# Kernel tuning notes

Measured on AMD Instinct MI355X. Metric: run time of the kernel, lower is better.

## Reference

```python
import jax, jax.numpy as jnp
import numpy as np

N = 50000      # nodes
E = 800000     # edges (avg degree 16)
F_IN = 64      # node_feature_dim
D = 128        # hidden_dim == output_dim
L = 3          # num_gnn_layers
B = 8          # number of graphs in the batch
GATE_H = 128   # GraphAttentionPool hidden_dim default


def _ln(x, g, b, eps=1e-5):
    m = x.mean(-1, keepdims=True)
    v = ((x - m) ** 2).mean(-1, keepdims=True)
    return (x - m) * jax.lax.rsqrt(v + eps) * g + b


def _gelu(x):
    return jax.nn.gelu(x, approximate=False)  # torch F.gelu default = exact erf


def setup_inputs() -> dict:
    key = jax.random.key(0)
    ks = jax.random.split(key, 12)
    p = lambda k, shape: (jax.random.normal(k, shape, jnp.float32) * 0.02)
    return {
        "x": jax.random.normal(ks[0], (N, F_IN), jnp.float32),
        "edge_index": jax.random.randint(ks[1], (2, E), 0, N, dtype=jnp.int32),
        "batch": jnp.sort(jax.random.randint(ks[2], (N,), 0, B, dtype=jnp.int32)),
        # input_proj: Linear + LayerNorm
        "w_in": p(ks[3], (F_IN, D)), "b_in": jnp.zeros((D,), jnp.float32),
        "ln_in_g": jnp.ones((D,), jnp.float32), "ln_in_b": jnp.zeros((D,), jnp.float32),
        # fallback GNN layers (stacked: all layers are 2D -> D)
        "gnn_w": p(ks[4], (L, 2 * D, D)), "gnn_b": jnp.zeros((L, D), jnp.float32),
        "gnn_ln_g": jnp.ones((L, D), jnp.float32), "gnn_ln_b": jnp.zeros((L, D), jnp.float32),
        # outer per-layer norms
        "norm_g": jnp.ones((L, D), jnp.float32), "norm_b": jnp.zeros((L, D), jnp.float32),
        # attention pool gate: Linear(D,128) -> tanh -> Linear(128,1)
        "gate_w1": p(ks[5], (D, GATE_H)), "gate_b1": jnp.zeros((GATE_H,), jnp.float32),
        "gate_w2": p(ks[6], (GATE_H,)), "gate_b2": jnp.zeros((), jnp.float32),
        # out_proj: Linear + LayerNorm + GELU
        "out_w": p(ks[7], (D, D)), "out_b": jnp.zeros((D,), jnp.float32),
        "out_ln_g": jnp.ones((D,), jnp.float32), "out_ln_b": jnp.zeros((D,), jnp.float32),
    }


def reference(x, edge_index, batch, w_in, b_in, ln_in_g, ln_in_b,
              gnn_w, gnn_b, gnn_ln_g, gnn_ln_b, norm_g, norm_b,
              gate_w1, gate_b1, gate_w2, gate_b2,
              out_w, out_b, out_ln_g, out_ln_b):
    src, dst = edge_index[0], edge_index[1]
    n = x.shape[0]

    # input_proj: Linear -> LayerNorm -> GELU
    h = _gelu(_ln(x @ w_in + b_in, ln_in_g, ln_in_b))

    # in-degree count (same every layer), clamped to >= 1
    deg = jax.ops.segment_sum(jnp.ones((src.shape[0],), h.dtype), dst, num_segments=n)
    deg = jnp.maximum(deg, 1.0)[:, None]  # (N, 1)

    for i in range(L):
        # mean-neighbor aggregation: gather x[src], scatter-add to dst
        agg = jax.ops.segment_sum(h[src], dst, num_segments=n) / deg  # (N, D)
        out = jnp.concatenate([h, agg], axis=-1) @ gnn_w[i] + gnn_b[i]
        h_new = _ln(_gelu(out), gnn_ln_g[i], gnn_ln_b[i])   # layer-internal norm
        h_new = _ln(h_new, norm_g[i], norm_b[i])             # outer norm
        if i < L - 1:
            h_new = _gelu(h_new) + h                         # residual (shapes match)
        h = h_new

    # attention pool (fallback path: global softmax over all nodes)
    gate_logits = jnp.tanh(h @ gate_w1 + gate_b1) @ gate_w2 + gate_b2  # (N,)
    gate = jax.nn.softmax(gate_logits, axis=0)
    pooled = jax.ops.segment_sum(h * gate[:, None], batch, num_segments=B)  # (B, D)

    spatial_embedding = _gelu(_ln(pooled @ out_w + out_b, out_ln_g, out_ln_b))
    return spatial_embedding, h, gate
```

## Files before the change

### kernel.cpp

```cpp
#include <hip/hip_runtime.h>
#include <math.h>

#define N_NODES 50000
#define N_EDGES 800000
#define F_IN 64
#define D 128
#define NLAYER 3
#define B_GRAPHS 8
#define GB 32
#define NPW 8
#define NBLK ((N_NODES + GB - 1) / GB)
#define SCAN_B 512
#define NPART ((N_NODES + SCAN_B - 1) / SCAN_B)
#define AGP 136

typedef float f32x4 __attribute__((ext_vector_type(4)));
typedef short bf16x8 __attribute__((ext_vector_type(8)));

__device__ __forceinline__ float gelu_exact(float x) {
    return 0.5f * x * (1.0f + erff(x * 0.7071067811865476f));
}

__device__ __forceinline__ unsigned short f2bf(float f) {
    unsigned int u = __float_as_uint(f);
    u = (u + 0x7fffu + ((u >> 16) & 1u)) >> 16;
    return (unsigned short)u;
}
__device__ __forceinline__ float bf2f(unsigned short u) {
    return __uint_as_float((unsigned int)u << 16);
}


__global__ void zero_int_kernel(int* __restrict__ p, int n) {
    int i = blockIdx.x * blockDim.x + threadIdx.x;
    int stride = gridDim.x * blockDim.x;
    for (; i < n; i += stride) p[i] = 0;
}

__global__ void degree_kernel(const int* __restrict__ dst, int* __restrict__ deg) {
    int e = blockIdx.x * blockDim.x + threadIdx.x;
    if (e < N_EDGES) atomicAdd(&deg[dst[e]], 1);
}

__global__ __launch_bounds__(SCAN_B) void scan_partials_kernel(const int* __restrict__ deg,
                                                               int* __restrict__ partials) {
    __shared__ int wsum[8];
    int tid = threadIdx.x;
    int lane = tid & 63, wave = tid >> 6;
    int i = blockIdx.x * SCAN_B + tid;
    int v = (i < N_NODES) ? deg[i] : 0;
    #pragma unroll
    for (int o = 32; o >= 1; o >>= 1) v += __shfl_xor(v, o);
    if (lane == 0) wsum[wave] = v;
    __syncthreads();
    if (tid == 0) {
        int t = 0;
        #pragma unroll
        for (int w = 0; w < 8; ++w) t += wsum[w];
        partials[blockIdx.x] = t;
    }
}

__global__ void scan_offsets_kernel(int* __restrict__ partials, int* __restrict__ row_ptr) {
    __shared__ int wtot[2];
    int tid = threadIdx.x;
    int lane = tid & 63, wave = tid >> 6;
    int v = (tid < NPART) ? partials[tid] : 0;
    int x = v;
    #pragma unroll
    for (int o = 1; o < 64; o <<= 1) { int nb = __shfl_up(x, o); if (lane >= o) x += nb; }
    if (lane == 63) wtot[wave] = x;
    __syncthreads();
    if (wave == 1) x += wtot[0];
    if (tid < NPART) partials[tid] = x - v;
    if (tid == 127) row_ptr[N_NODES] = x;
}

__global__ __launch_bounds__(SCAN_B) void scan_apply_kernel(const int* __restrict__ deg,
        const int* __restrict__ partials, int* __restrict__ row_ptr, int* __restrict__ cursor) {
    __shared__ int wsum[8];
    int tid = threadIdx.x;
    int lane = tid & 63, wave = tid >> 6;
    int i = blockIdx.x * SCAN_B + tid;
    int v = (i < N_NODES) ? deg[i] : 0;
    int x = v;
    #pragma unroll
    for (int o = 1; o < 64; o <<= 1) { int nb = __shfl_up(x, o); if (lane >= o) x += nb; }
    if (lane == 63) wsum[wave] = x;
    __syncthreads();
    int waveoff = 0;
    #pragma unroll
    for (int w = 0; w < 8; ++w) waveoff += (w < wave) ? wsum[w] : 0;
    int excl = partials[blockIdx.x] + waveoff + x - v;
    if (i < N_NODES) { row_ptr[i] = excl; cursor[i] = excl; }
}

__global__ void fill_kernel(const int* __restrict__ src, const int* __restrict__ dst,
                            int* __restrict__ cursor, int* __restrict__ csr) {
    int e = blockIdx.x * blockDim.x + threadIdx.x;
    if (e < N_EDGES) {
        int t = dst[e];
        int pos = atomicAdd(&cursor[t], 1);
        csr[pos] = src[e];
    }
}

#define WT_GNN (NLAYER * D * 2 * D)
#define WT_G1  (WT_GNN + D * D)
#define WT_ALL (WT_G1 + D * F_IN)
__global__ void wprep_kernel(const float* __restrict__ gnn_w, const float* __restrict__ gate_w1,
                             const float* __restrict__ w_in, unsigned short* __restrict__ wt,
                             float* __restrict__ pooled) {
    int idx = blockIdx.x * 256 + threadIdx.x;
    if (blockIdx.x == 0) {
        #pragma unroll
        for (int i = 0; i < 4; ++i) pooled[threadIdx.x + i * 256] = 0.f;
    }
    if (idx >= WT_ALL) return;
    if (idx < WT_GNN) {
        int l = idx / (D * 2 * D);
        int rem = idx - l * (D * 2 * D);
        int n = rem / (2 * D);
        int k = rem - n * (2 * D);
        wt[idx] = f2bf(gnn_w[(size_t)l * 2 * D * D + (size_t)k * D + n]);
    } else if (idx < WT_G1) {
        int rem = idx - WT_GNN;
        int n = rem / D;
        int k = rem - n * D;
        wt[idx] = f2bf(gate_w1[(size_t)k * D + n]);
    } else {
        int rem = idx - WT_G1;
        int n = rem / F_IN;
        int k = rem - n * F_IN;
        wt[idx] = f2bf(w_in[(size_t)k * D + n]);
    }
}


__global__ __launch_bounds__(256) void input_proj_v5(
        const float* __restrict__ x, const unsigned short* __restrict__ wti,
        const float* __restrict__ b, const float* __restrict__ gam,
        const float* __restrict__ bet, unsigned short* __restrict__ h16) {
    __shared__ float2 red[2][GB];
    int tid = threadIdx.x;
    int wave = tid >> 6, lane = tid & 63;
    int nblk0 = blockIdx.x * GB;
    int q = lane >> 4, c = lane & 15;
    int m0 = (wave >> 1) * 16;
    int n0 = (wave & 1) * 64;
    int mrow = nblk0 + m0 + c;
    int mclamp = (mrow < N_NODES) ? mrow : (N_NODES - 1);
    const float* xr = x + (size_t)mclamp * F_IN;

    f32x4 acc[4];
    #pragma unroll
    for (int t = 0; t < 4; ++t) {
        float bn = b[n0 + t * 16 + c];
        acc[t] = (f32x4){bn, bn, bn, bn};
    }
    #pragma unroll
    for (int kk = 0; kk < 2; ++kk) {
        float4 a0 = *(const float4*)&xr[kk * 32 + q * 8];
        float4 a1 = *(const float4*)&xr[kk * 32 + q * 8 + 4];
        bf16x8 av;
        av[0] = (short)f2bf(a0.x); av[1] = (short)f2bf(a0.y);
        av[2] = (short)f2bf(a0.z); av[3] = (short)f2bf(a0.w);
        av[4] = (short)f2bf(a1.x); av[5] = (short)f2bf(a1.y);
        av[6] = (short)f2bf(a1.z); av[7] = (short)f2bf(a1.w);
        #pragma unroll
        for (int t = 0; t < 4; ++t) {
            bf16x8 bv = *(const bf16x8*)&wti[(size_t)(n0 + t * 16 + c) * F_IN + kk * 32 + q * 8];
            acc[t] = __builtin_amdgcn_mfma_f32_16x16x32_bf16(av, bv, acc[t], 0, 0, 0);
        }
    }
    float s[4], sq[4];
    #pragma unroll
    for (int r = 0; r < 4; ++r) {
        s[r] = acc[0][r] + acc[1][r] + acc[2][r] + acc[3][r];
        sq[r] = acc[0][r] * acc[0][r] + acc[1][r] * acc[1][r]
              + acc[2][r] * acc[2][r] + acc[3][r] * acc[3][r];
    }
    #pragma unroll
    for (int o = 1; o <= 8; o <<= 1)
        #pragma unroll
        for (int r = 0; r < 4; ++r) { s[r] += __shfl_xor(s[r], o); sq[r] += __shfl_xor(sq[r], o); }
    if (c == 0) {
        #pragma unroll
        for (int r = 0; r < 4; ++r) red[wave & 1][m0 + q * 4 + r] = make_float2(s[r], sq[r]);
    }
    __syncthreads();
    float gv[4], bv2[4];
    #pragma unroll
    for (int t = 0; t < 4; ++t) {
        int nn = n0 + t * 16 + c;
        gv[t] = gam[nn]; bv2[t] = bet[nn];
    }
    #pragma unroll
    for (int r = 0; r < 4; ++r) {
        int m = m0 + q * 4 + r;
        int n = nblk0 + m;
        float2 p0 = red[0][m], p1 = red[1][m];
        float mean = (p0.x + p1.x) * (1.0f / D);
        float msq  = (p0.y + p1.y) * (1.0f / D);
        float istd = rsqrtf(msq - mean * mean + 1e-5f);
        if (n < N_NODES) {
            #pragma unroll
            for (int t = 0; t < 4; ++t) {
                int nn = n0 + t * 16 + c;
                float y = (acc[t][r] - mean) * istd * gv[t] + bv2[t];
                h16[(size_t)n * D + nn] = f2bf(gelu_exact(y));
            }
        }
    }
}


__device__ __forceinline__ void acc_row(float acc[8], bf16x8 v) {
    #pragma unroll
    for (int i = 0; i < 8; ++i)
        acc[i] += __uint_as_float(((unsigned int)(unsigned short)v[i]) << 16);
}

template<int DO_GATE>
__global__ __launch_bounds__(256) void gnn_layer_v7(
        const unsigned short* __restrict__ h16_in, unsigned short* __restrict__ h16_out,
        float* __restrict__ hf_out,
        const int* __restrict__ csr, const int* __restrict__ rp,
        const unsigned short* __restrict__ wt,
        const float* __restrict__ bias,
        const float* __restrict__ ln1g, const float* __restrict__ ln1b,
        const float* __restrict__ ln2g, const float* __restrict__ ln2b,
        int residual, int write_f32,
        const unsigned short* __restrict__ wtg,
        const float* __restrict__ gb1, const float* __restrict__ gw2,
        const float* __restrict__ gb2,
        float* __restrict__ logits, float2* __restrict__ gpart) {
    __shared__ int rps[GB + 1];
    __shared__ int eidx[GB][32];
    __shared__ unsigned short aggb[GB][AGP];
    __shared__ float2 red1[2][GB];
    __shared__ float2 red2[2][GB];
    __shared__ float redg[2][GB];
    __shared__ float lg[GB];

    int tid = threadIdx.x;
    int wave = tid >> 6, lane = tid & 63;
    int nblk0 = blockIdx.x * GB;
    int gbase = wave * NPW;

    if (tid < GB + 1) {
        int n = nblk0 + tid;
        if (n > N_NODES) n = N_NODES;
        rps[tid] = rp[n];
    }
    __syncthreads();
    #pragma unroll
    for (int k2 = 0; k2 < 4; ++k2) {
        int f = tid + k2 * 256;
        int g = f >> 5, sl = f & 31;
        int beg = rps[g], end = rps[g + 1];
        int ee = beg + sl;
        int ci = (ee < end) ? ee : ((end > beg) ? (end - 1) : 0);
        eidx[g][sl] = csr[ci];
    }
    __syncthreads();

    {
        int er = lane >> 4, dg = lane & 15;
        #pragma unroll
        for (int j = 0; j < NPW; ++j) {
            int g = gbase + j;
            int beg = rps[g], end = rps[g + 1];
            int deg = end - beg;
            int id8[8];
            #pragma unroll
            for (int t = 0; t < 8; ++t) id8[t] = eidx[g][er + 4 * t];
            bf16x8 v[8];
            #pragma unroll
            for (int t = 0; t < 8; ++t)
                v[t] = *(const bf16x8*)&h16_in[(size_t)id8[t] * D + dg * 8];
            float acc[8];
            #pragma unroll
            for (int i = 0; i < 8; ++i) acc[i] = 0.f;
            #pragma unroll
            for (int t = 0; t < 8; ++t)
                if (beg + er + 4 * t < end) acc_row(acc, v[t]);
            if (deg > 32) {
                for (int ee = beg + er + 32; ee < end; ee += 4) {
                    bf16x8 vv = *(const bf16x8*)&h16_in[(size_t)csr[ee] * D + dg * 8];
                    acc_row(acc, vv);
                }
            }
            #pragma unroll
            for (int i = 0; i < 8; ++i) {
                acc[i] += __shfl_xor(acc[i], 16);
                acc[i] += __shfl_xor(acc[i], 32);
            }
            float inv = 1.0f / fmaxf((float)deg, 1.0f);
            if (er == 0) {
                bf16x8 o;
                #pragma unroll
                for (int i = 0; i < 8; ++i) o[i] = (short)f2bf(acc[i] * inv);
                *(bf16x8*)&aggb[g][dg * 8] = o;
            }
        }
    }
    __syncthreads();

    int q = lane >> 4, c = lane & 15;
    int m0 = (wave >> 1) * 16;
    int n0 = (wave & 1) * 64;
    int mrow = nblk0 + m0 + c;
    int mclamp = (mrow < N_NODES) ? mrow : (N_NODES - 1);
    const unsigned short* arow = h16_in + (size_t)mclamp * D;

    f32x4 acc[4];
    #pragma unroll
    for (int t = 0; t < 4; ++t) {
        float bn = bias[n0 + t * 16 + c];
        acc[t] = (f32x4){bn, bn, bn, bn};
    }
    #pragma unroll
    for (int kk = 0; kk < 4; ++kk) {
        bf16x8 av = *(const bf16x8*)&arow[kk * 32 + q * 8];
        #pragma unroll
        for (int t = 0; t < 4; ++t) {
            bf16x8 bv = *(const bf16x8*)&wt[(size_t)(n0 + t * 16 + c) * 256 + kk * 32 + q * 8];
            acc[t] = __builtin_amdgcn_mfma_f32_16x16x32_bf16(av, bv, acc[t], 0, 0, 0);
        }
    }
    #pragma unroll
    for (int kk = 0; kk < 4; ++kk) {
        bf16x8 av = *(const bf16x8*)&aggb[m0 + c][kk * 32 + q * 8];
        #pragma unroll
        for (int t = 0; t < 4; ++t) {
            bf16x8 bv = *(const bf16x8*)&wt[(size_t)(n0 + t * 16 + c) * 256 + 128 + kk * 32 + q * 8];
            acc[t] = __builtin_amdgcn_mfma_f32_16x16x32_bf16(av, bv, acc[t], 0, 0, 0);
        }
    }

    float xv[4][4];
    #pragma unroll
    for (int t = 0; t < 4; ++t)
        #pragma unroll
        for (int r = 0; r < 4; ++r) xv[t][r] = gelu_exact(acc[t][r]);

    float s[4], sq[4];
    #pragma unroll
    for (int r = 0; r < 4; ++r) {
        s[r] = xv[0][r] + xv[1][r] + xv[2][r] + xv[3][r];
        sq[r] = xv[0][r] * xv[0][r] + xv[1][r] * xv[1][r] + xv[2][r] * xv[2][r] + xv[3][r] * xv[3][r];
    }
    #pragma unroll
    for (int o = 1; o <= 8; o <<= 1)
        #pragma unroll
        for (int r = 0; r < 4; ++r) { s[r] += __shfl_xor(s[r], o); sq[r] += __shfl_xor(sq[r], o); }
    int nh = wave & 1;
    if (c == 0) {
        #pragma unroll
        for (int r = 0; r < 4; ++r) red1[nh][m0 + q * 4 + r] = make_float2(s[r], sq[r]);
    }
    __syncthreads();

    float g1v[4], b1v[4], g2v[4], b2v[4];
    #pragma unroll
    for (int t = 0; t < 4; ++t) {
        int nn = n0 + t * 16 + c;
        g1v[t] = ln1g[nn]; b1v[t] = ln1b[nn];
        g2v[t] = ln2g[nn]; b2v[t] = ln2b[nn];
    }

    float y1[4][4];
    #pragma unroll
    for (int r = 0; r < 4; ++r) {
        int m = m0 + q * 4 + r;
        float2 p0 = red1[0][m], p1 = red1[1][m];
        float mean = (p0.x + p1.x) * (1.0f / D);
        float msq  = (p0.y + p1.y) * (1.0f / D);
        float istd = rsqrtf(msq - mean * mean + 1e-5f);
        #pragma unroll
        for (int t = 0; t < 4; ++t)
            y1[t][r] = (xv[t][r] - mean) * istd * g1v[t] + b1v[t];
    }

    #pragma unroll
    for (int r = 0; r < 4; ++r) {
        s[r] = y1[0][r] + y1[1][r] + y1[2][r] + y1[3][r];
        sq[r] = y1[0][r] * y1[0][r] + y1[1][r] * y1[1][r] + y1[2][r] * y1[2][r] + y1[3][r] * y1[3][r];
    }
    #pragma unroll
    for (int o = 1; o <= 8; o <<= 1)
        #pragma unroll
        for (int r = 0; r < 4; ++r) { s[r] += __shfl_xor(s[r], o); sq[r] += __shfl_xor(sq[r], o); }
    if (c == 0) {
        #pragma unroll
        for (int r = 0; r < 4; ++r) red2[nh][m0 + q * 4 + r] = make_float2(s[r], sq[r]);
    }
    __syncthreads();

    #pragma unroll
    for (int r = 0; r < 4; ++r) {
        int m = m0 + q * 4 + r;
        int n = nblk0 + m;
        float2 p0 = red2[0][m], p1 = red2[1][m];
        float mean = (p0.x + p1.x) * (1.0f / D);
        float msq  = (p0.y + p1.y) * (1.0f / D);
        float istd = rsqrtf(msq - mean * mean + 1e-5f);
        #pragma unroll
        for (int t = 0; t < 4; ++t) {
            int nn = n0 + t * 16 + c;
            float y2 = (y1[t][r] - mean) * istd * g2v[t] + b2v[t];
            float o = residual ? (gelu_exact(y2) + bf2f(h16_in[(size_t)n * D + nn])) : y2;
            if (n < N_NODES) {
                h16_out[(size_t)n * D + nn] = f2bf(o);
                if (write_f32) hf_out[(size_t)n * D + nn] = o;
            }
            if (DO_GATE) aggb[m][nn] = f2bf(o);
        }
    }

    if (DO_GATE) {
        __syncthreads();
        f32x4 gacc[4];
        #pragma unroll
        for (int t = 0; t < 4; ++t) {
            float bn = gb1[n0 + t * 16 + c];
            gacc[t] = (f32x4){bn, bn, bn, bn};
        }
        #pragma unroll
        for (int kk = 0; kk < 4; ++kk) {
            bf16x8 av = *(const bf16x8*)&aggb[m0 + c][kk * 32 + q * 8];
            #pragma unroll
            for (int t = 0; t < 4; ++t) {
                bf16x8 bv = *(const bf16x8*)&wtg[(size_t)(n0 + t * 16 + c) * 128 + kk * 32 + q * 8];
                gacc[t] = __builtin_amdgcn_mfma_f32_16x16x32_bf16(av, bv, gacc[t], 0, 0, 0);
            }
        }
        float w2v[4];
        #pragma unroll
        for (int t = 0; t < 4; ++t) w2v[t] = gw2[n0 + t * 16 + c];
        float gs[4];
        #pragma unroll
        for (int r = 0; r < 4; ++r) {
            gs[r] = tanhf(gacc[0][r]) * w2v[0] + tanhf(gacc[1][r]) * w2v[1]
                  + tanhf(gacc[2][r]) * w2v[2] + tanhf(gacc[3][r]) * w2v[3];
        }
        #pragma unroll
        for (int o = 1; o <= 8; o <<= 1)
            #pragma unroll
            for (int r = 0; r < 4; ++r) gs[r] += __shfl_xor(gs[r], o);
        if (c == 0) {
            #pragma unroll
            for (int r = 0; r < 4; ++r) redg[nh][m0 + q * 4 + r] = gs[r];
        }
        __syncthreads();
        if ((wave & 1) == 0 && c == 0) {
            float bb2 = gb2[0];
            #pragma unroll
            for (int r = 0; r < 4; ++r) {
                int m = m0 + q * 4 + r;
                int n = nblk0 + m;
                float L = redg[0][m] + redg[1][m] + bb2;
                if (n < N_NODES) { logits[n] = L; lg[m] = L; }
                else lg[m] = -INFINITY;
            }
        }
        __syncthreads();
        if (wave == 0) {
            float l = (lane < GB) ? lg[lane] : -INFINITY;
            float mx = l;
            #pragma unroll
            for (int o = 32; o >= 1; o >>= 1) mx = fmaxf(mx, __shfl_xor(mx, o));
            float ex = (lane < GB && l > -INFINITY) ? expf(l - mx) : 0.f;
            #pragma unroll
            for (int o = 32; o >= 1; o >>= 1) ex += __shfl_xor(ex, o);
            if (lane == 0) gpart[blockIdx.x] = make_float2(mx, ex);
        }
    }
}


#define POOL_CHUNK 128
__global__ __launch_bounds__(POOL_CHUNK) void gate_pool_v2(
        const unsigned short* __restrict__ h16, const float* __restrict__ logits,
        const float2* __restrict__ gpart, const int* __restrict__ batch,
        float* __restrict__ gate_out, float* __restrict__ pooled) {
    __shared__ float sb[4];
    __shared__ float gs[POOL_CHUNK];
    __shared__ int bs[POOL_CHUNK];
    int d = threadIdx.x;
    int lane = d & 63, wv = d >> 6;
    float mx = -INFINITY;
    for (int i = d; i < NBLK; i += POOL_CHUNK) mx = fmaxf(mx, gpart[i].x);
    #pragma unroll
    for (int o = 32; o >= 1; o >>= 1) mx = fmaxf(mx, __shfl_xor(mx, o));
    if (lane == 0) sb[wv] = mx;
    __syncthreads();
    mx = fmaxf(sb[0], sb[1]);
    float ssum = 0.f;
    for (int i = d; i < NBLK; i += POOL_CHUNK) {
        float2 p = gpart[i];
        ssum += p.y * expf(p.x - mx);
    }
    #pragma unroll
    for (int o = 32; o >= 1; o >>= 1) ssum += __shfl_xor(ssum, o);
    if (lane == 0) sb[2 + wv] = ssum;
    __syncthreads();
    float inv = 1.0f / (sb[2] + sb[3]);

    int n0 = blockIdx.x * POOL_CHUNK;
    int nj = n0 + d;
    if (nj < N_NODES) {
        float gv = expf(logits[nj] - mx) * inv;
        gs[d] = gv;
        bs[d] = batch[nj];
        gate_out[nj] = gv;
    }
    __syncthreads();
    int count = min(POOL_CHUNK, N_NODES - n0);
    float acc = 0.f;
    int cur = bs[0];
    int t = 0;
    for (; t + 3 < count; t += 4) {
        float h0 = bf2f(h16[(size_t)(n0 + t + 0) * D + d]);
        float h1 = bf2f(h16[(size_t)(n0 + t + 1) * D + d]);
        float h2 = bf2f(h16[(size_t)(n0 + t + 2) * D + d]);
        float h3 = bf2f(h16[(size_t)(n0 + t + 3) * D + d]);
        int b0 = bs[t], b1 = bs[t + 1], b2 = bs[t + 2], b3 = bs[t + 3];
        if (b0 != cur) { atomicAdd(&pooled[cur * D + d], acc); acc = 0.f; cur = b0; }
        acc = fmaf(h0, gs[t], acc);
        if (b1 != cur) { atomicAdd(&pooled[cur * D + d], acc); acc = 0.f; cur = b1; }
        acc = fmaf(h1, gs[t + 1], acc);
        if (b2 != cur) { atomicAdd(&pooled[cur * D + d], acc); acc = 0.f; cur = b2; }
        acc = fmaf(h2, gs[t + 2], acc);
        if (b3 != cur) { atomicAdd(&pooled[cur * D + d], acc); acc = 0.f; cur = b3; }
        acc = fmaf(h3, gs[t + 3], acc);
    }
    for (; t < count; ++t) {
        int bn = bs[t];
        if (bn != cur) { atomicAdd(&pooled[cur * D + d], acc); acc = 0.f; cur = bn; }
        acc = fmaf(bf2f(h16[(size_t)(n0 + t) * D + d]), gs[t], acc);
    }
    atomicAdd(&pooled[cur * D + d], acc);
}

__global__ void out_proj_kernel(const float* __restrict__ pooled, const float* __restrict__ w,
                                const float* __restrict__ b, const float* __restrict__ g,
                                const float* __restrict__ beta, float* __restrict__ emb) {
    __shared__ float ps[D];
    __shared__ float sbuf[2];
    int bg = blockIdx.x, d = threadIdx.x;
    ps[d] = pooled[bg * D + d];
    __syncthreads();
    float acc = b[d];
    #pragma unroll 8
    for (int k = 0; k < D; ++k) acc += ps[k] * w[k * D + d];
    float s = acc, q = acc * acc;
    #pragma unroll
    for (int o = 32; o >= 1; o >>= 1) { s += __shfl_down(s, o); q += __shfl_down(q, o); }
    if ((d & 63) == 0) { sbuf[d >> 6] = s; }
    __syncthreads();
    float fullsum = sbuf[0] + sbuf[1];
    __syncthreads();
    if ((d & 63) == 0) { sbuf[d >> 6] = q; }
    __syncthreads();
    float fullsq = sbuf[0] + sbuf[1];
    float m = fullsum * (1.0f / D);
    float var = fullsq * (1.0f / D) - m * m;
    float y = (acc - m) * rsqrtf(var + 1e-5f) * g[d] + beta[d];
    emb[bg * D + d] = gelu_exact(y);
}

extern "C" void kernel_launch(void* const* d_in, const int* in_sizes, int n_in,
                              void* d_out, int out_size, void* d_ws, size_t ws_size,
                              hipStream_t stream) {
    const float* x        = (const float*)d_in[0];
    const int*   edge     = (const int*)d_in[1];
    const int*   batch    = (const int*)d_in[2];
    const float* w_in     = (const float*)d_in[3];
    const float* b_in     = (const float*)d_in[4];
    const float* ln_in_g  = (const float*)d_in[5];
    const float* ln_in_b  = (const float*)d_in[6];
    const float* gnn_w    = (const float*)d_in[7];
    const float* gnn_b    = (const float*)d_in[8];
    const float* gnn_ln_g = (const float*)d_in[9];
    const float* gnn_ln_b = (const float*)d_in[10];
    const float* norm_g   = (const float*)d_in[11];
    const float* norm_b   = (const float*)d_in[12];
    const float* gate_w1  = (const float*)d_in[13];
    const float* gate_b1  = (const float*)d_in[14];
    const float* gate_w2  = (const float*)d_in[15];
    const float* gate_b2  = (const float*)d_in[16];
    const float* out_w    = (const float*)d_in[17];
    const float* out_b    = (const float*)d_in[18];
    const float* out_ln_g = (const float*)d_in[19];
    const float* out_ln_b = (const float*)d_in[20];

    const int* src = edge;
    const int* dst = edge + N_EDGES;

    float* out      = (float*)d_out;
    float* emb      = out;
    float* hA       = out + B_GRAPHS * D;
    float* gate_out = hA + (size_t)N_NODES * D;

    unsigned short* h16A = (unsigned short*)d_ws;
    unsigned short* h16B = h16A + (size_t)N_NODES * D;
    int*   deg_i    = (int*)d_ws;
    int*   cursor   = (int*)d_ws + N_NODES;
    int*   row_ptr  = (int*)(h16B + (size_t)N_NODES * D);
    int*   csr      = row_ptr + N_NODES + 1;
    float* logits   = (float*)(csr + N_EDGES);
    float* pooled   = logits + N_NODES;
    int*   partials = (int*)(pooled + B_GRAPHS * D);
    float2* gpart   = (float2*)(((uintptr_t)(partials + NPART) + 15) & ~(uintptr_t)15);
    unsigned short* wt  = (unsigned short*)(gpart + NBLK);
    unsigned short* wtg = wt + WT_GNN;
    unsigned short* wti = wt + WT_G1;

    zero_int_kernel<<<128, 256, 0, stream>>>(deg_i, N_NODES);
    degree_kernel<<<(N_EDGES + 255) / 256, 256, 0, stream>>>(dst, deg_i);
    scan_partials_kernel<<<NPART, SCAN_B, 0, stream>>>(deg_i, partials);
    scan_offsets_kernel<<<1, 128, 0, stream>>>(partials, row_ptr);
    scan_apply_kernel<<<NPART, SCAN_B, 0, stream>>>(deg_i, partials, row_ptr, cursor);
    fill_kernel<<<(N_EDGES + 255) / 256, 256, 0, stream>>>(src, dst, cursor, csr);
    wprep_kernel<<<(WT_ALL + 255) / 256, 256, 0, stream>>>(gnn_w, gate_w1, w_in, wt, pooled);

    input_proj_v5<<<NBLK, 256, 0, stream>>>(x, wti, b_in, ln_in_g, ln_in_b, h16B);

    gnn_layer_v7<0><<<NBLK, 256, 0, stream>>>(
        h16B, h16A, hA, csr, row_ptr, wt, gnn_b,
        gnn_ln_g, gnn_ln_b, norm_g, norm_b, 1, 0,
        nullptr, nullptr, nullptr, nullptr, nullptr, nullptr);
    gnn_layer_v7<0><<<NBLK, 256, 0, stream>>>(
        h16A, h16B, hA, csr, row_ptr, wt + (size_t)1 * D * 2 * D, gnn_b + D,
        gnn_ln_g + D, gnn_ln_b + D, norm_g + D, norm_b + D, 1, 0,
        nullptr, nullptr, nullptr, nullptr, nullptr, nullptr);
    gnn_layer_v7<1><<<NBLK, 256, 0, stream>>>(
        h16B, h16A, hA, csr, row_ptr, wt + (size_t)2 * D * 2 * D, gnn_b + 2 * D,
        gnn_ln_g + 2 * D, gnn_ln_b + 2 * D, norm_g + 2 * D, norm_b + 2 * D, 0, 1,
        wtg, gate_b1, gate_w2, gate_b2, logits, gpart);

    gate_pool_v2<<<(N_NODES + POOL_CHUNK - 1) / POOL_CHUNK, POOL_CHUNK, 0, stream>>>(
        h16A, logits, gpart, batch, gate_out, pooled);
    out_proj_kernel<<<B_GRAPHS, D, 0, stream>>>(pooled, out_w, out_b, out_ln_g, out_ln_b, emb);
}
```

Before: 455.6 us.

## Interleave two-node gathers, fuse scan offsets, memset degrees, halve pool chunk

The neighbor aggregation now processes two nodes per iteration, issuing both nodes' sixteen gathered row loads before accumulating, so more memory requests are in flight. The scan-offsets kernel is removed: each apply block sums the preceding partials itself, and block 0 writes the total. The zeroing kernel becomes a hipMemsetAsync. The gate-pool kernel uses 64-node chunks per block to double the block count. The price is more registers in the gather loop, which may lower occupancy, plus redundant partial sums in the scan.

New measurement: 458.8 us. Within noise of the previous version (+0.7%).

```diff
diff --git a/kernel.cpp b/kernel.cpp
--- a/kernel.cpp
+++ b/kernel.cpp
@@ -31,12 +31,6 @@
 }
 
 
-__global__ void zero_int_kernel(int* __restrict__ p, int n) {
-    int i = blockIdx.x * blockDim.x + threadIdx.x;
-    int stride = gridDim.x * blockDim.x;
-    for (; i < n; i += stride) p[i] = 0;
-}
-
 __global__ void degree_kernel(const int* __restrict__ dst, int* __restrict__ deg) {
     int e = blockIdx.x * blockDim.x + threadIdx.x;
     if (e < N_EDGES) atomicAdd(&deg[dst[e]], 1);
@@ -61,26 +55,45 @@
     }
 }
 
-__global__ void scan_offsets_kernel(int* __restrict__ partials, int* __restrict__ row_ptr) {
-    __shared__ int wtot[2];
+__global__ __launch_bounds__(SCAN_B) void scan_apply_v2(const int* __restrict__ deg,
+        const int* __restrict__ partials, int* __restrict__ row_ptr, int* __restrict__ cursor) {
+    __shared__ int wsum[8];
+    __shared__ int base_s;
     int tid = threadIdx.x;
     int lane = tid & 63, wave = tid >> 6;
-    int v = (tid < NPART) ? partials[tid] : 0;
-    int x = v;
-    #pragma unroll
-    for (int o = 1; o < 64; o <<= 1) { int nb = __shfl_up(x, o); if (lane >= o) x += nb; }
-    if (lane == 63) wtot[wave] = x;
-    __syncthreads();
-    if (wave == 1) x += wtot[0];
-    if (tid < NPART) partials[tid] = x - v;
-    if (tid == 127) row_ptr[N_NODES] = x;
-}
-
-__global__ __launch_bounds__(SCAN_B) void scan_apply_kernel(const int* __restrict__ deg,
-        const int* __restrict__ partials, int* __restrict__ row_ptr, int* __restrict__ cursor) {
-    __shared__ int wsum[8];
-    int tid = threadIdx.x;
-    int lane = tid & 63, wave = tid >> 6;
+
+    int b = 0;
+    for (int i = tid; i < (int)blockIdx.x; i += SCAN_B) b += partials[i];
+    #pragma unroll
+    for (int o = 32; o >= 1; o >>= 1) b += __shfl_xor(b, o);
+    if (lane == 0) wsum[wave] = b;
+    __syncthreads();
+    if (tid == 0) {
+        int t = 0;
+        #pragma unroll
+        for (int w = 0; w < 8; ++w) t += wsum[w];
+        base_s = t;
+    }
+    __syncthreads();
+    int base = base_s;
+    __syncthreads();
+
+    if (blockIdx.x == 0) {
+        int t = 0;
+        for (int i = tid; i < NPART; i += SCAN_B) t += partials[i];
+        #pragma unroll
+        for (int o = 32; o >= 1; o >>= 1) t += __shfl_xor(t, o);
+        if (lane == 0) wsum[wave] = t;
+        __syncthreads();
+        if (tid == 0) {
+            int tt = 0;
+            #pragma unroll
+            for (int w = 0; w < 8; ++w) tt += wsum[w];
+            row_ptr[N_NODES] = tt;
+        }
+        __syncthreads();
+    }
+
     int i = blockIdx.x * SCAN_B + tid;
     int v = (i < N_NODES) ? deg[i] : 0;
     int x = v;
@@ -91,7 +104,7 @@
     int waveoff = 0;
     #pragma unroll
     for (int w = 0; w < 8; ++w) waveoff += (w < wave) ? wsum[w] : 0;
-    int excl = partials[blockIdx.x] + waveoff + x - v;
+    int excl = base + waveoff + x - v;
     if (i < N_NODES) { row_ptr[i] = excl; cursor[i] = excl; }
 }
 
@@ -222,7 +235,7 @@
 }
 
 template<int DO_GATE>
-__global__ __launch_bounds__(256) void gnn_layer_v7(
+__global__ __launch_bounds__(256) void gnn_layer_v8(
         const unsigned short* __restrict__ h16_in, unsigned short* __restrict__ h16_out,
         float* __restrict__ hf_out,
         const int* __restrict__ csr, const int* __restrict__ rp,
@@ -268,40 +281,61 @@
     {
         int er = lane >> 4, dg = lane & 15;
         #pragma unroll
-        for (int j = 0; j < NPW; ++j) {
-            int g = gbase + j;
-            int beg = rps[g], end = rps[g + 1];
-            int deg = end - beg;
-            int id8[8];
-            #pragma unroll
-            for (int t = 0; t < 8; ++t) id8[t] = eidx[g][er + 4 * t];
-            bf16x8 v[8];
+        for (int jj = 0; jj < NPW; jj += 2) {
+            int gA = gbase + jj, gB2 = gbase + jj + 1;
+            int begA = rps[gA], endA = rps[gA + 1];
+            int begB = rps[gB2], endB = rps[gB2 + 1];
+            int degA = endA - begA, degB = endB - begB;
+            int idA[8], idB[8];
+            #pragma unroll
+            for (int t = 0; t < 8; ++t) { idA[t] = eidx[gA][er + 4 * t]; idB[t] = eidx[gB2][er + 4 * t]; }
+            bf16x8 vA[8], vB[8];
             #pragma unroll
             for (int t = 0; t < 8; ++t)
-                v[t] = *(const bf16x8*)&h16_in[(size_t)id8[t] * D + dg * 8];
-            float acc[8];
-            #pragma unroll
-            for (int i = 0; i < 8; ++i) acc[i] = 0.f;
+                vA[t] = *(const bf16x8*)&h16_in[(size_t)idA[t] * D + dg * 8];
             #pragma unroll
             for (int t = 0; t < 8; ++t)
-                if (beg + er + 4 * t < end) acc_row(acc, v[t]);
-            if (deg > 32) {
-                for (int ee = beg + er + 32; ee < end; ee += 4) {
+                vB[t] = *(const bf16x8*)&h16_in[(size_t)idB[t] * D + dg * 8];
+
+            float accA[8], accB[8];
+            #pragma unroll
+            for (int i = 0; i < 8; ++i) { accA[i] = 0.f; accB[i] = 0.f; }
+            #pragma unroll
+            for (int t = 0; t < 8; ++t)
+                if (begA + er + 4 * t < endA) acc_row(accA, vA[t]);
+            #pragma unroll
+            for (int t = 0; t < 8; ++t)
+                if (begB + er + 4 * t < endB) acc_row(accB, vB[t]);
+            if (degA > 32) {
+                for (int ee = begA + er + 32; ee < endA; ee += 4) {
                     bf16x8 vv = *(const bf16x8*)&h16_in[(size_t)csr[ee] * D + dg * 8];
-                    acc_row(acc, vv);
+                    acc_row(accA, vv);
                 }
             }
+            if (degB > 32) {
+                for (int ee = begB + er + 32; ee < endB; ee += 4) {
+                    bf16x8 vv = *(const bf16x8*)&h16_in[(size_t)csr[ee] * D + dg * 8];
+                    acc_row(accB, vv);
+                }
+            }
             #pragma unroll
             for (int i = 0; i < 8; ++i) {
-                acc[i] += __shfl_xor(acc[i], 16);
-                acc[i] += __shfl_xor(acc[i], 32);
-            }
-            float inv = 1.0f / fmaxf((float)deg, 1.0f);
+                accA[i] += __shfl_xor(accA[i], 16);
+                accA[i] += __shfl_xor(accA[i], 32);
+                accB[i] += __shfl_xor(accB[i], 16);
+                accB[i] += __shfl_xor(accB[i], 32);
+            }
+            float invA = 1.0f / fmaxf((float)degA, 1.0f);
+            float invB = 1.0f / fmaxf((float)degB, 1.0f);
             if (er == 0) {
-                bf16x8 o;
+                bf16x8 oA, oB;
                 #pragma unroll
-                for (int i = 0; i < 8; ++i) o[i] = (short)f2bf(acc[i] * inv);
-                *(bf16x8*)&aggb[g][dg * 8] = o;
+                for (int i = 0; i < 8; ++i) {
+                    oA[i] = (short)f2bf(accA[i] * invA);
+                    oB[i] = (short)f2bf(accB[i] * invB);
+                }
+                *(bf16x8*)&aggb[gA][dg * 8] = oA;
+                *(bf16x8*)&aggb[gB2][dg * 8] = oB;
             }
         }
     }
@@ -480,25 +514,25 @@
 }
 
 
-#define POOL_CHUNK 128
-__global__ __launch_bounds__(POOL_CHUNK) void gate_pool_v2(
+#define PC 64
+__global__ __launch_bounds__(128) void gate_pool_v3(
         const unsigned short* __restrict__ h16, const float* __restrict__ logits,
         const float2* __restrict__ gpart, const int* __restrict__ batch,
         float* __restrict__ gate_out, float* __restrict__ pooled) {
     __shared__ float sb[4];
-    __shared__ float gs[POOL_CHUNK];
-    __shared__ int bs[POOL_CHUNK];
+    __shared__ float gs[PC];
+    __shared__ int bs[PC];
     int d = threadIdx.x;
     int lane = d & 63, wv = d >> 6;
     float mx = -INFINITY;
-    for (int i = d; i < NBLK; i += POOL_CHUNK) mx = fmaxf(mx, gpart[i].x);
+    for (int i = d; i < NBLK; i += 128) mx = fmaxf(mx, gpart[i].x);
     #pragma unroll
     for (int o = 32; o >= 1; o >>= 1) mx = fmaxf(mx, __shfl_xor(mx, o));
     if (lane == 0) sb[wv] = mx;
     __syncthreads();
     mx = fmaxf(sb[0], sb[1]);
     float ssum = 0.f;
-    for (int i = d; i < NBLK; i += POOL_CHUNK) {
+    for (int i = d; i < NBLK; i += 128) {
         float2 p = gpart[i];
         ssum += p.y * expf(p.x - mx);
     }
@@ -508,16 +542,18 @@
     __syncthreads();
     float inv = 1.0f / (sb[2] + sb[3]);
 
-    int n0 = blockIdx.x * POOL_CHUNK;
-    int nj = n0 + d;
-    if (nj < N_NODES) {
-        float gv = expf(logits[nj] - mx) * inv;
-        gs[d] = gv;
-        bs[d] = batch[nj];
-        gate_out[nj] = gv;
-    }
-    __syncthreads();
-    int count = min(POOL_CHUNK, N_NODES - n0);
+    int n0 = blockIdx.x * PC;
+    if (d < PC) {
+        int nj = n0 + d;
+        if (nj < N_NODES) {
+            float gv = expf(logits[nj] - mx) * inv;
+            gs[d] = gv;
+            bs[d] = batch[nj];
+            gate_out[nj] = gv;
+        }
+    }
+    __syncthreads();
+    int count = min(PC, N_NODES - n0);
     float acc = 0.f;
     int cur = bs[0];
     int t = 0;
@@ -618,30 +654,29 @@
     unsigned short* wtg = wt + WT_GNN;
     unsigned short* wti = wt + WT_G1;
 
-    zero_int_kernel<<<128, 256, 0, stream>>>(deg_i, N_NODES);
+    hipMemsetAsync(deg_i, 0, N_NODES * sizeof(int), stream);
     degree_kernel<<<(N_EDGES + 255) / 256, 256, 0, stream>>>(dst, deg_i);
     scan_partials_kernel<<<NPART, SCAN_B, 0, stream>>>(deg_i, partials);
-    scan_offsets_kernel<<<1, 128, 0, stream>>>(partials, row_ptr);
-    scan_apply_kernel<<<NPART, SCAN_B, 0, stream>>>(deg_i, partials, row_ptr, cursor);
+    scan_apply_v2<<<NPART, SCAN_B, 0, stream>>>(deg_i, partials, row_ptr, cursor);
     fill_kernel<<<(N_EDGES + 255) / 256, 256, 0, stream>>>(src, dst, cursor, csr);
     wprep_kernel<<<(WT_ALL + 255) / 256, 256, 0, stream>>>(gnn_w, gate_w1, w_in, wt, pooled);
 
     input_proj_v5<<<NBLK, 256, 0, stream>>>(x, wti, b_in, ln_in_g, ln_in_b, h16B);
 
-    gnn_layer_v7<0><<<NBLK, 256, 0, stream>>>(
+    gnn_layer_v8<0><<<NBLK, 256, 0, stream>>>(
         h16B, h16A, hA, csr, row_ptr, wt, gnn_b,
         gnn_ln_g, gnn_ln_b, norm_g, norm_b, 1, 0,
         nullptr, nullptr, nullptr, nullptr, nullptr, nullptr);
-    gnn_layer_v7<0><<<NBLK, 256, 0, stream>>>(
+    gnn_layer_v8<0><<<NBLK, 256, 0, stream>>>(
         h16A, h16B, hA, csr, row_ptr, wt + (size_t)1 * D * 2 * D, gnn_b + D,
         gnn_ln_g + D, gnn_ln_b + D, norm_g + D, norm_b + D, 1, 0,
         nullptr, nullptr, nullptr, nullptr, nullptr, nullptr);
-    gnn_layer_v7<1><<<NBLK, 256, 0, stream>>>(
+    gnn_layer_v8<1><<<NBLK, 256, 0, stream>>>(
         h16B, h16A, hA, csr, row_ptr, wt + (size_t)2 * D * 2 * D, gnn_b + 2 * D,
         gnn_ln_g + 2 * D, gnn_ln_b + 2 * D, norm_g + 2 * D, norm_b + 2 * D, 0, 1,
         wtg, gate_b1, gate_w2, gate_b2, logits, gpart);
 
-    gate_pool_v2<<<(N_NODES + POOL_CHUNK - 1) / POOL_CHUNK, POOL_CHUNK, 0, stream>>>(
+    gate_pool_v3<<<(N_NODES + PC - 1) / PC, 128, 0, stream>>>(
         h16A, logits, gpart, batch, gate_out, pooled);
     out_proj_kernel<<<B_GRAPHS, D, 0, stream>>>(pooled, out_w, out_b, out_ln_g, out_ln_b, emb);
 }
```
